# Performance work log

Measured on AMD Instinct MI355X. Metric: run time of the kernel, lower is better.

The kernel has to match this reference:

```python
import jax, jax.numpy as jnp
import numpy as np

B, L, T = 16, 256, 256
ENC, DEC, MEL, SPK = 256, 1024, 80, 256
ATT, FILT, K = 128, 32, 31


def setup_inputs() -> dict:
    key = jax.random.key(0)
    ks = jax.random.split(key, 32)
    s = 0.05
    r = lambda k, shape: jax.random.normal(k, shape, dtype=jnp.float32) * s
    return {
        'encoder_outputs': jax.random.normal(ks[0], (B, L, ENC), dtype=jnp.float32),
        'speaker_embed': jax.random.normal(ks[1], (B, SPK), dtype=jnp.float32),
        'mels': jax.random.normal(ks[2], (B, T, MEL), dtype=jnp.float32),
        # prenet
        'W_pre1': r(ks[3], (DEC, MEL)), 'b_pre1': jnp.zeros((DEC,), jnp.float32),
        'W_pre2': r(ks[4], (DEC, DEC)), 'b_pre2': jnp.zeros((DEC,), jnp.float32),
        # speaker projection
        'W_sp': r(ks[5], (DEC, SPK)), 'b_sp': jnp.zeros((DEC,), jnp.float32),
        # location-sensitive attention (Tacotron-2 style)
        'W_q': r(ks[6], (ATT, DEC)),
        'W_m': r(ks[7], (ATT, ENC)),
        'W_loc_conv': r(ks[8], (FILT, 2, K)),
        'W_loc': r(ks[9], (ATT, FILT)),
        'v_att': r(ks[10], (ATT,)),
        # LSTM cells
        'W_ih1': r(ks[11], (4 * DEC, DEC + ENC)), 'W_hh1': r(ks[12], (4 * DEC, DEC)),
        'b_ih1': jnp.zeros((4 * DEC,), jnp.float32), 'b_hh1': jnp.zeros((4 * DEC,), jnp.float32),
        'W_ih2': r(ks[13], (4 * DEC, DEC)), 'W_hh2': r(ks[14], (4 * DEC, DEC)),
        'b_ih2': jnp.zeros((4 * DEC,), jnp.float32), 'b_hh2': jnp.zeros((4 * DEC,), jnp.float32),
        # output projections
        'W_mel': r(ks[15], (MEL, DEC)), 'b_mel': jnp.zeros((MEL,), jnp.float32),
        'W_stop': r(ks[16], (1, DEC)), 'b_stop': jnp.zeros((1,), jnp.float32),
    }


def _lstm_cell(x, h, c, W_ih, W_hh, b_ih, b_hh):
    g = x @ W_ih.T + h @ W_hh.T + b_ih + b_hh
    i, f, gg, o = jnp.split(g, 4, axis=-1)
    c2 = jax.nn.sigmoid(f) * c + jax.nn.sigmoid(i) * jnp.tanh(gg)
    h2 = jax.nn.sigmoid(o) * jnp.tanh(c2)
    return h2, c2


def reference(encoder_outputs, speaker_embed, mels,
              W_pre1, b_pre1, W_pre2, b_pre2, W_sp, b_sp,
              W_q, W_m, W_loc_conv, W_loc, v_att,
              W_ih1, W_hh1, b_ih1, b_hh1, W_ih2, W_hh2, b_ih2, b_hh2,
              W_mel, b_mel, W_stop, b_stop):
    b = encoder_outputs.shape[0]
    proc_mem = jnp.einsum('bld,ad->bla', encoder_outputs, W_m)  # [B,L,ATT]
    spk = speaker_embed @ W_sp.T + b_sp                          # [B,DEC]
    # teacher forcing: step 0 uses zeros, step i>0 uses mels[:, i] (matches torch loop)
    prev_mel_seq = jnp.concatenate([jnp.zeros_like(mels[:, :1]), mels[:, 1:]], axis=1)
    prev_mel_seq = prev_mel_seq.transpose(1, 0, 2)               # [T,B,MEL]

    def step(carry, prev_mel):
        h1, c1, h2, c2, prev_w, cum_w = carry
        # prenet (dropout = identity in eval)
        p = jax.nn.relu(prev_mel @ W_pre1.T + b_pre1)
        p = jax.nn.relu(p @ W_pre2.T + b_pre2)
        q = p + spk
        # location features over [prev, cumulative] attention weights
        loc = jnp.stack([prev_w, cum_w], axis=1)                 # [B,2,L]
        f = jax.lax.conv_general_dilated(loc, W_loc_conv, (1,), [(K // 2, K // 2)],
                                         dimension_numbers=('NCH', 'OIH', 'NCH'))  # [B,FILT,L]
        e = jnp.einsum('bla,a->bl', jnp.tanh((q @ W_q.T)[:, None, :]
                                             + jnp.einsum('bcl,ac->bla', f, W_loc)
                                             + proc_mem), v_att)  # [B,L]
        w = jax.nn.softmax(e, axis=1)
        ctx = jnp.einsum('bl,bld->bd', w, encoder_outputs)        # [B,ENC]
        h1n, c1n = _lstm_cell(jnp.concatenate([p, ctx], axis=1), h1, c1, W_ih1, W_hh1, b_ih1, b_hh1)
        h2n, c2n = _lstm_cell(h1n, h2, c2, W_ih2, W_hh2, b_ih2, b_hh2)
        mel = h2n @ W_mel.T + b_mel
        stop = jax.nn.sigmoid(h2n @ W_stop.T + b_stop)
        return (h1n, c1n, h2n, c2n, w, cum_w + w), (mel, stop)

    z = lambda d: jnp.zeros((b, d), jnp.float32)
    carry0 = (z(DEC), z(DEC), z(DEC), z(DEC), z(L), z(L))
    _, (mel_seq, stop_seq) = jax.lax.scan(step, carry0, prev_mel_seq)
    return mel_seq.transpose(1, 0, 2), stop_seq.transpose(1, 0, 2)
```

## Files before the change

kernel.cpp:

```cpp
#include <hip/hip_runtime.h>


namespace {

constexpr int TT = 256, BB = 16, LL = 256, MELD = 80, FILTD = 32, KC = 31;
constexpr int P1 = 2304;
constexpr int P2 = 2048;
constexpr int REDOFF = 32768;

typedef float f32x4 __attribute__((ext_vector_type(4)));

struct Args {
  const float *enc, *spe, *mels;
  const float *Wpre1, *bpre1, *Wpre2, *bpre2, *Wsp, *bsp;
  const float *Wq, *Wm, *Wconv, *Wloc, *vatt;
  const float *Wih1, *Whh1, *bih1, *bhh1;
  const float *Wih2, *Whh2, *bih2, *bhh2;
  const float *Wmel, *bmel, *Wstop, *bstop;
  float *p, *X, *qp2, *pm2, *prevmel;
  float *h1a, *h1b, *c1, *h2a, *h2b, *c2;
  float *cum, *wexp, *uctx, *pctx, *psum, *spkvec, *spkq;
  float *W81, *b81, *tmp;
  int *slots, *epoch, *pslots, *pepoch;
  float *out;
};

__device__ __forceinline__ float fast_tanh(float x) {
  float ax = fabsf(x);
  float e = __expf(-2.f * ax);
  float t = (1.f - e) / (1.f + e);
  return copysignf(t, x);
}
__device__ __forceinline__ float fast_sig(float x) { return 1.f / (1.f + __expf(-x)); }

__device__ __forceinline__ int cldi(const int* p) {
  int v;
  asm volatile("global_load_dword %0, %1, off sc0 sc1\n\ts_waitcnt vmcnt(0)"
               : "=v"(v) : "v"(p) : "memory");
  return v;
}
__device__ __forceinline__ void cst1(float* p, float v) {
  asm volatile("global_store_dword %0, %1, off sc0 sc1" :: "v"(p), "v"(v) : "memory");
}
__device__ __forceinline__ void csti(int* p, int v) {
  asm volatile("global_store_dword %0, %1, off sc0 sc1" :: "v"(p), "v"(v) : "memory");
}
__device__ __forceinline__ void cld2(float* d0, float* d1, const float* q0,
                                     const float* q1) {
  float x, y;
  asm volatile(
      "global_load_dword %0, %2, off sc0 sc1\n\t"
      "global_load_dword %1, %3, off sc0 sc1\n\t"
      "s_waitcnt vmcnt(0)"
      : "=&v"(x), "=&v"(y) : "v"(q0), "v"(q1) : "memory");
  *d0 = x; *d1 = y;
}
__device__ __forceinline__ void cld4(f32x4 d[4], const f32x4* q0, const f32x4* q1,
                                     const f32x4* q2, const f32x4* q3) {
  asm volatile(
      "global_load_dwordx4 %0, %4, off sc0 sc1\n\t"
      "global_load_dwordx4 %1, %5, off sc0 sc1\n\t"
      "global_load_dwordx4 %2, %6, off sc0 sc1\n\t"
      "global_load_dwordx4 %3, %7, off sc0 sc1\n\t"
      "s_waitcnt vmcnt(0)"
      : "=&v"(d[0]), "=&v"(d[1]), "=&v"(d[2]), "=&v"(d[3])
      : "v"(q0), "v"(q1), "v"(q2), "v"(q3)
      : "memory");
}
__device__ __forceinline__ void cld8d(float d[8], const float* q0, const float* q1,
                                      const float* q2, const float* q3, const float* q4,
                                      const float* q5, const float* q6, const float* q7) {
  asm volatile(
      "global_load_dword %0, %8, off sc0 sc1\n\t"
      "global_load_dword %1, %9, off sc0 sc1\n\t"
      "global_load_dword %2, %10, off sc0 sc1\n\t"
      "global_load_dword %3, %11, off sc0 sc1\n\t"
      "global_load_dword %4, %12, off sc0 sc1\n\t"
      "global_load_dword %5, %13, off sc0 sc1\n\t"
      "global_load_dword %6, %14, off sc0 sc1\n\t"
      "global_load_dword %7, %15, off sc0 sc1\n\t"
      "s_waitcnt vmcnt(0)"
      : "=&v"(d[0]), "=&v"(d[1]), "=&v"(d[2]), "=&v"(d[3]),
        "=&v"(d[4]), "=&v"(d[5]), "=&v"(d[6]), "=&v"(d[7])
      : "v"(q0), "v"(q1), "v"(q2), "v"(q3), "v"(q4), "v"(q5), "v"(q6), "v"(q7)
      : "memory");
}

__device__ __forceinline__ void bar_lgkm() {
  asm volatile("s_waitcnt lgkmcnt(0)" ::: "memory");
  __builtin_amdgcn_s_barrier();
  __builtin_amdgcn_sched_barrier(0);
}

__device__ __forceinline__ void glls_c(const float* g, float* l) {
  __builtin_amdgcn_global_load_lds((const __attribute__((address_space(1))) void*)g,
                                   (__attribute__((address_space(3))) void*)l, 16, 0, 17);
}
__device__ __forceinline__ void glls_p(const float* g, float* l) {
  __builtin_amdgcn_global_load_lds((const __attribute__((address_space(1))) void*)g,
                                   (__attribute__((address_space(3))) void*)l, 16, 0, 0);
}

__device__ __forceinline__ void gridbar(int* slots, int* epoch, int target) {
  __syncthreads();
  if (blockIdx.x == 0) {
    if (threadIdx.x == 0) csti(&slots[0], target);
    while (cldi(&slots[threadIdx.x * 32]) < target) __builtin_amdgcn_s_sleep(1);
    __syncthreads();
    if (threadIdx.x == 0) csti(epoch, target);
  } else {
    if (threadIdx.x == 0) {
      csti(&slots[blockIdx.x * 32], target);
      while (cldi(epoch) < target) __builtin_amdgcn_s_sleep(8);
    }
  }
  __syncthreads();
}

__global__ void k_init(float* base, int n) {
  int i = blockIdx.x * blockDim.x + threadIdx.x;
  if (i < n) base[i] = 0.f;
}

__global__ void k_setpsum(float* psum) {
  if (threadIdx.x < 16) psum[256 + threadIdx.x * 16] = 1.f;
}

__global__ void k_prevmel(Args a) {
  int i = blockIdx.x * blockDim.x + threadIdx.x;
  if (i >= TT * BB * MELD) return;
  int m = i % MELD;
  int tb = i / MELD;
  int b = tb & 15, t = tb >> 4;
  a.prevmel[i] = (t == 0) ? 0.f : a.mels[(b * TT + t) * MELD + m];
}

__global__ void k_spkvec(Args a) {
  int i = blockIdx.x * blockDim.x + threadIdx.x;
  if (i >= BB * 1024) return;
  int b = i >> 10, j = i & 1023;
  const float* x = a.spe + b * 256;
  const float* w = a.Wsp + j * 256;
  float s = a.bsp[j];
  for (int k = 0; k < 256; ++k) s += x[k] * w[k];
  a.spkvec[i] = s;
}

__global__ void k_spkq(Args a) {
  int i = blockIdx.x * blockDim.x + threadIdx.x;
  if (i >= BB * 128) return;
  int b = i >> 7, q = i & 127;
  const float* x = a.spkvec + b * 1024;
  const float* w = a.Wq + q * 1024;
  float s = 0.f;
  for (int k = 0; k < 1024; ++k) s += x[k] * w[k];
  a.spkq[i] = s;
}

__global__ void k_prep81(Args a) {
  int i = blockIdx.x * blockDim.x + threadIdx.x;
  if (i < 81 * 1024) {
    int r = i >> 10, k = i & 1023;
    a.W81[i] = (r < 80) ? a.Wmel[r * 1024 + k] : a.Wstop[k];
  }
  if (i < 81) a.b81[i] = (i < 80) ? a.bmel[i] : a.bstop[0];
}

__global__ __launch_bounds__(256) void k_gemm(const float* __restrict__ A,
                                              const float* __restrict__ Bm,
                                              const float* __restrict__ bias,
                                              float* __restrict__ C,
                                              int M, int N, int K, int act) {
  __shared__ __align__(16) float As[16][132];
  __shared__ __align__(16) float Bs[16][68];
  const int bm = blockIdx.y * 128, bn = blockIdx.x * 64;
  const int tid = threadIdx.x;
  const int tm = (tid >> 4) * 8, tn = (tid & 15) * 4;
  float acc[8][4] = {};
  for (int k0 = 0; k0 < K; k0 += 16) {
    for (int i = tid; i < 512; i += 256) {
      int m = i >> 2, kq = i & 3;
      float4 v = *(const float4*)(A + (size_t)(bm + m) * K + k0 + kq * 4);
      As[kq * 4 + 0][m] = v.x; As[kq * 4 + 1][m] = v.y;
      As[kq * 4 + 2][m] = v.z; As[kq * 4 + 3][m] = v.w;
    }
    {
      int m = tid >> 2, kq = tid & 3;
      float4 v = *(const float4*)(Bm + (size_t)(bn + m) * K + k0 + kq * 4);
      Bs[kq * 4 + 0][m] = v.x; Bs[kq * 4 + 1][m] = v.y;
      Bs[kq * 4 + 2][m] = v.z; Bs[kq * 4 + 3][m] = v.w;
    }
    __syncthreads();
#pragma unroll
    for (int kk = 0; kk < 16; ++kk) {
      float4 a0 = *(const float4*)&As[kk][tm];
      float4 a1 = *(const float4*)&As[kk][tm + 4];
      float4 b0 = *(const float4*)&Bs[kk][tn];
      float av[8] = {a0.x, a0.y, a0.z, a0.w, a1.x, a1.y, a1.z, a1.w};
      float bv[4] = {b0.x, b0.y, b0.z, b0.w};
#pragma unroll
      for (int i = 0; i < 8; ++i)
#pragma unroll
        for (int j = 0; j < 4; ++j) acc[i][j] += av[i] * bv[j];
    }
    __syncthreads();
  }
#pragma unroll
  for (int i = 0; i < 8; ++i)
#pragma unroll
    for (int j = 0; j < 4; ++j) {
      float v = acc[i][j];
      if (bias) v += bias[bn + tn + j];
      if (act == 1) v = fmaxf(v, 0.f);
      C[(size_t)(bm + tm + i) * N + bn + tn + j] = v;
    }
}

__global__ void k_pm_transpose(Args a) {
  int i = blockIdx.x * blockDim.x + threadIdx.x;
  if (i >= BB * 128 * LL) return;
  int l = i & 255;
  int rest = i >> 8;
  int q = rest & 127, b = rest >> 7;
  a.pm2[i] = a.X[(size_t)((b << 8) + l) * 128 + q];
}

__global__ void k_addspkq(Args a) {
  int i = blockIdx.x * blockDim.x + threadIdx.x;
  if (i >= TT * BB * 128) return;
  int q = i & 127, b = (i >> 7) & 15;
  a.qp2[i] += a.spkq[b * 128 + q];
}

__global__ __launch_bounds__(256, 1) void k_persist(Args a) {
  __shared__ __align__(16) float xs[16 * P1];
  __shared__ __align__(16) float asc[720];
  __shared__ __align__(16) float gbuf2[280];
  __shared__ __align__(16) float wfb[2048];
  const int wg = blockIdx.x, tid = threadIdx.x;
  const int wv = tid >> 6, lane = tid & 63;
  const int d0 = wg * 4, kl = lane * 4;
  const int ag = tid & 15, ll = tid >> 4;

  float* loc0 = asc;
  float* loc1 = asc + 64;
  float* aF   = asc + 128;
  float* expv = asc + 704;

  float4 wL1[9][4];
  float4 wL2[8][4];
#pragma unroll
  for (int q = 0; q < 4; ++q) {
    const int row = wv * 1024 + d0 + q;
    const float* rih1 = a.Wih1 + (size_t)row * 1280;
    const float* rhh1 = a.Whh1 + (size_t)row * 1024;
    const float* rih2 = a.Wih2 + (size_t)row * 1024;
    const float* rhh2 = a.Whh2 + (size_t)row * 1024;
#pragma unroll
    for (int kb = 0; kb < 9; ++kb)
      wL1[kb][q] = (kb < 5) ? *(const float4*)(rih1 + kb * 256 + kl)
                            : *(const float4*)(rhh1 + kb * 256 + kl - 1280);
#pragma unroll
    for (int kb = 0; kb < 8; ++kb)
      wL2[kb][q] = (kb < 4) ? *(const float4*)(rih2 + kb * 256 + kl)
                            : *(const float4*)(rhh2 + kb * 256 + kl - 1024);
  }
  const int row_r = wv * 1024 + d0 + (lane >> 4);
  const float bsum1 = a.bih1[row_r] + a.bhh1[row_r];
  const float bsum2 = a.bih2[row_r] + a.bhh2[row_r];

  const int bH = wg >> 4, cH = wg & 15, l0H = cH << 4, lH = l0H + ll;
  float pmv[8], va[8];
  {
    const float* pmb = a.pm2 + (size_t)bH * 32768;
#pragma unroll
    for (int j = 0; j < 8; ++j) {
      pmv[j] = pmb[(size_t)(ag * 8 + j) * 256 + lH];
      va[j] = a.vatt[ag * 8 + j];
    }
  }
  float ev[16];
  {
    const float* eb = a.enc + (size_t)((bH << 8) + l0H) * 256 + tid;
#pragma unroll
    for (int l2 = 0; l2 < 16; ++l2) ev[l2] = eb[l2 * 256];
  }

  float c1v = 0.f, c2v = 0.f;
  __syncthreads();

  for (int t = 0; t < 259; ++t) {
    const int cur = t & 1, prv = cur ^ 1;

    if (wg < 16 && t >= 1 && t <= 256) {
      const int par = (t - 1) & 1, b = wg;
      float sm;
      {
        const f32x4* ps4 = (const f32x4*)(a.psum + par * 256 + b * 16);
        f32x4 pd[4];
        cld4(pd, ps4, ps4 + 1, ps4 + 2, ps4 + 3);
        sm = 0.f;
#pragma unroll
        for (int i = 0; i < 4; ++i) sm += pd[i][0] + pd[i][1] + pd[i][2] + pd[i][3];
      }
      const float inv = 1.f / sm;
      const float* pc = a.pctx + par * 65536 + b * 4096 + tid;
      float d[8];
      float acc = 0.f;
      cld8d(d, pc, pc + 256, pc + 512, pc + 768, pc + 1024, pc + 1280, pc + 1536,
            pc + 1792);
#pragma unroll
      for (int i = 0; i < 8; ++i) acc += d[i];
      cld8d(d, pc + 2048, pc + 2304, pc + 2560, pc + 2816, pc + 3072, pc + 3328,
            pc + 3584, pc + 3840);
#pragma unroll
      for (int i = 0; i < 8; ++i) acc += d[i];
      cst1(a.uctx + par * 4096 + b * 256 + tid, acc * inv);
    }

    float qv[8];
    if (t < 256) {
      float sm;
      {
        const f32x4* ps4 = (const f32x4*)(a.psum + prv * 256 + bH * 16);
        f32x4 pd[4];
        cld4(pd, ps4, ps4 + 1, ps4 + 2, ps4 + 3);
        sm = 0.f;
#pragma unroll
        for (int i = 0; i < 4; ++i) sm += pd[i][0] + pd[i][1] + pd[i][2] + pd[i][3];
      }
      const float inv_ps = 1.f / sm;
      {
        const float* qpb = a.qp2 + ((size_t)(t << 4) + bH) * 128 + ag * 8;
        *(float4*)&qv[0] = *(const float4*)qpb;
        *(float4*)&qv[4] = *(const float4*)(qpb + 4);
      }
      if (tid < 64) {
        int lp = l0H - 16 + tid;
        bool ok = (lp >= 0 && lp < LL);
        float we = 0.f, cm = 0.f;
        if (ok)
          cld2(&we, &cm, a.wexp + prv * 4096 + bH * 256 + lp,
               a.cum + prv * 4096 + bH * 256 + lp);
        float wn = we * inv_ps;
        loc0[tid] = wn;
        loc1[tid] = ok ? (cm + wn) : 0.f;
      }
      bar_lgkm();
      if (tid < 16) cst1(a.cum + cur * 4096 + bH * 256 + l0H + tid, loc1[16 + tid]);
      for (int idx = tid; idx < FILTD * 16; idx += 256) {
        int fc = idx >> 4, ll2 = idx & 15;
        const float* w = a.Wconv + fc * 62;
        float s = 0.f;
#pragma unroll
        for (int k = 0; k < KC; ++k) {
          s += w[k] * loc0[ll2 + k + 1];
          s += w[31 + k] * loc1[ll2 + k + 1];
        }
        aF[ll2 * 36 + fc] = s;
      }
      bar_lgkm();
      {
        const float* ftr = aF + ll * 36;
#pragma unroll
        for (int j = 0; j < 8; ++j) {
          const int r = ag * 8 + j;
          const float* wl = a.Wloc + r * 32;
          float x = 0.f;
#pragma unroll
          for (int c4 = 0; c4 < 8; ++c4) {
            float4 w4 = *(const float4*)(wl + c4 * 4);
            f32x4 f4 = *(const f32x4*)(ftr + c4 * 4);
            x += w4.x * f4[0] + w4.y * f4[1] + w4.z * f4[2] + w4.w * f4[3];
          }
          wfb[r * 16 + ll] = x;
        }
      }
    }

    if (t >= 2 && t <= 257) {
      const int s1 = t - 2;
      const float* pt = a.p + (size_t)s1 * 16384;
      const float* h1r = (s1 & 1) ? a.h1a : a.h1b;
      const float* uc = a.uctx + (size_t)(s1 & 1) * 4096;
#pragma unroll
      for (int k = 0; k < 16; ++k)
        glls_p(pt + (size_t)(tid + k * 256) * 4, xs + k * P1 + wv * 256);
#pragma unroll
      for (int k = 0; k < 4; ++k)
        glls_c(uc + (size_t)(tid + k * 256) * 4, xs + (k * 4 + wv) * P1 + 1024);
#pragma unroll
      for (int k = 0; k < 16; ++k)
        glls_c(h1r + (size_t)(tid + k * 256) * 4, xs + k * P1 + 1280 + wv * 256);
    }

    if (t < 256) {
      bar_lgkm();
      {
        float s = 0.f;
#pragma unroll
        for (int j = 0; j < 8; ++j) {
          float x = qv[j] + pmv[j] + wfb[(ag * 8 + j) * 16 + ll];
          s += va[j] * fast_tanh(x);
        }
        s += __shfl_down(s, 8, 16);
        s += __shfl_down(s, 4, 16);
        s += __shfl_down(s, 2, 16);
        s += __shfl_down(s, 1, 16);
        if (ag == 0) {
          float ex = __expf(s);
          expv[ll] = ex;
          cst1(a.wexp + cur * 4096 + bH * 256 + lH, ex);
        }
      }
      bar_lgkm();
      if (tid == 0) {
        float s = 0.f;
#pragma unroll
        for (int i = 0; i < 16; ++i) s += expv[i];
        cst1(a.psum + cur * 256 + bH * 16 + cH, s);
      }
      {
        float sctx = 0.f;
#pragma unroll
        for (int l2 = 0; l2 < 16; ++l2) sctx += expv[l2] * ev[l2];
        cst1(a.pctx + cur * 65536 + (bH * 16 + cH) * 256 + tid, sctx);
      }
    }

    if (t >= 2 && t <= 257) {
      __syncthreads();
      float acc[4][16];
#pragma unroll
      for (int q = 0; q < 4; ++q)
#pragma unroll
        for (int b = 0; b < 16; ++b) acc[q][b] = 0.f;
#pragma unroll
      for (int kb = 0; kb < 9; ++kb) {
        const float* xb = xs + kb * 256 + kl;
#pragma unroll
        for (int b = 0; b < 16; ++b) {
          float4 x4 = *(const float4*)(xb + b * P1);
#pragma unroll
          for (int q = 0; q < 4; ++q) {
            acc[q][b] += wL1[kb][q].x * x4.x;
            acc[q][b] += wL1[kb][q].y * x4.y;
            acc[q][b] += wL1[kb][q].z * x4.z;
            acc[q][b] += wL1[kb][q].w * x4.w;
          }
        }
      }
#pragma unroll
      for (int q = 0; q < 4; ++q)
#pragma unroll
        for (int b = 0; b < 16; ++b) {
          float v = acc[q][b];
          v += __shfl_xor(v, 32);
          v += __shfl_xor(v, 16);
          acc[q][b] = v;
        }
      if (lane < 16) {
        float* rb = xs + REDOFF + wv * 1024 + lane * 64;
        const int sx = lane << 2;
#pragma unroll
        for (int q = 0; q < 4; ++q)
#pragma unroll
          for (int bg = 0; bg < 4; ++bg) {
            f32x4 v = {acc[q][bg * 4 + 0], acc[q][bg * 4 + 1],
                       acc[q][bg * 4 + 2], acc[q][bg * 4 + 3]};
            *(f32x4*)(rb + ((q * 16 + bg * 4) ^ sx)) = v;
          }
      }
    }
    bar_lgkm();

    if (t >= 3) {
      const int s2 = t - 3;
      const float* h1s = (s2 & 1) ? a.h1b : a.h1a;
      const float* h2r = (s2 & 1) ? a.h2a : a.h2b;
#pragma unroll
      for (int k = 0; k < 16; ++k)
        glls_c(h1s + (size_t)(tid + k * 256) * 4, xs + k * P2 + wv * 256);
#pragma unroll
      for (int k = 0; k < 16; ++k)
        glls_c(h2r + (size_t)(tid + k * 256) * 4, xs + k * P2 + 1024 + wv * 256);
    }

    if (t >= 2 && t <= 257) {
      float* h1w = ((t - 2) & 1) ? a.h1b : a.h1a;
      {
        const int lo = lane & ~3, li = lane & 3;
        const float* rbase = xs + REDOFF + wv * 1024;
        float g = bsum1;
#pragma unroll
        for (int k = 0; k < 16; ++k) g += rbase[k * 64 + (lo ^ (k << 2)) + li];
        gbuf2[wv * 68 + lane] = g;
      }
      bar_lgkm();
      if (tid < 64) {
        int dd = tid >> 4, b = tid & 15, d = d0 + dd;
        float gi = gbuf2[0 * 68 + tid], gf = gbuf2[1 * 68 + tid];
        float gg = gbuf2[2 * 68 + tid], go = gbuf2[3 * 68 + tid];
        float cn = fast_sig(gf) * c1v + fast_sig(gi) * fast_tanh(gg);
        float hn = fast_sig(go) * fast_tanh(cn);
        c1v = cn;
        cst1(h1w + b * 1024 + d, hn);
      }
    }

    if (t >= 3) {
      const int s2 = t - 3;
      float* h2w = (s2 & 1) ? a.h2b : a.h2a;
      __syncthreads();
      float acc[4][16];
#pragma unroll
      for (int q = 0; q < 4; ++q)
#pragma unroll
        for (int b = 0; b < 16; ++b) acc[q][b] = 0.f;
#pragma unroll
      for (int kb = 0; kb < 8; ++kb) {
        const float* xb = xs + kb * 256 + kl;
#pragma unroll
        for (int b = 0; b < 16; ++b) {
          float4 x4 = *(const float4*)(xb + b * P2);
#pragma unroll
          for (int q = 0; q < 4; ++q) {
            acc[q][b] += wL2[kb][q].x * x4.x;
            acc[q][b] += wL2[kb][q].y * x4.y;
            acc[q][b] += wL2[kb][q].z * x4.z;
            acc[q][b] += wL2[kb][q].w * x4.w;
          }
        }
      }
#pragma unroll
      for (int q = 0; q < 4; ++q)
#pragma unroll
        for (int b = 0; b < 16; ++b) {
          float v = acc[q][b];
          v += __shfl_xor(v, 32);
          v += __shfl_xor(v, 16);
          acc[q][b] = v;
        }
      if (lane < 16) {
        float* rb = xs + REDOFF + wv * 1024 + lane * 64;
        const int sx = lane << 2;
#pragma unroll
        for (int q = 0; q < 4; ++q)
#pragma unroll
          for (int bg = 0; bg < 4; ++bg) {
            f32x4 v = {acc[q][bg * 4 + 0], acc[q][bg * 4 + 1],
                       acc[q][bg * 4 + 2], acc[q][bg * 4 + 3]};
            *(f32x4*)(rb + ((q * 16 + bg * 4) ^ sx)) = v;
          }
      }
      bar_lgkm();
      {
        const int lo = lane & ~3, li = lane & 3;
        const float* rbase = xs + REDOFF + wv * 1024;
        float g = bsum2;
#pragma unroll
        for (int k = 0; k < 16; ++k) g += rbase[k * 64 + (lo ^ (k << 2)) + li];
        gbuf2[wv * 68 + lane] = g;
      }
      bar_lgkm();
      if (tid < 64) {
        int dd = tid >> 4, b = tid & 15, d = d0 + dd;
        float gi = gbuf2[0 * 68 + tid], gf = gbuf2[1 * 68 + tid];
        float gg = gbuf2[2 * 68 + tid], go = gbuf2[3 * 68 + tid];
        float cn = fast_sig(gf) * c2v + fast_sig(gi) * fast_tanh(gg);
        float hn = fast_sig(go) * fast_tanh(cn);
        c2v = cn;
        cst1(h2w + b * 1024 + d, hn);
        a.X[(size_t)(s2 * 16 + b) * 1024 + d] = hn;
      }
    }

    if (t < 258) gridbar(a.slots, a.epoch, t + 1);
  }
}

__global__ void k_finish(Args a) {
  int i = blockIdx.x * blockDim.x + threadIdx.x;
  if (i >= 4096 * 128) return;
  int col = i & 127, tb = i >> 7;
  int t = tb >> 4, b = tb & 15;
  float v = a.tmp[i];
  if (col < 80) a.out[(size_t)(b * 256 + t) * 80 + col] = v;
  else if (col == 80) a.out[327680 + b * 256 + t] = fast_sig(v);
}

}

extern "C" void kernel_launch(void* const* d_in, const int* in_sizes, int n_in,
                              void* d_out, int out_size, void* d_ws, size_t ws_size,
                              hipStream_t stream) {
  float* ws = (float*)d_ws;
  Args a;
  a.enc = (const float*)d_in[0];
  a.spe = (const float*)d_in[1];
  a.mels = (const float*)d_in[2];
  a.Wpre1 = (const float*)d_in[3];  a.bpre1 = (const float*)d_in[4];
  a.Wpre2 = (const float*)d_in[5];  a.bpre2 = (const float*)d_in[6];
  a.Wsp = (const float*)d_in[7];    a.bsp = (const float*)d_in[8];
  a.Wq = (const float*)d_in[9];     a.Wm = (const float*)d_in[10];
  a.Wconv = (const float*)d_in[11]; a.Wloc = (const float*)d_in[12];
  a.vatt = (const float*)d_in[13];
  a.Wih1 = (const float*)d_in[14];  a.Whh1 = (const float*)d_in[15];
  a.bih1 = (const float*)d_in[16];  a.bhh1 = (const float*)d_in[17];
  a.Wih2 = (const float*)d_in[18];  a.Whh2 = (const float*)d_in[19];
  a.bih2 = (const float*)d_in[20];  a.bhh2 = (const float*)d_in[21];
  a.Wmel = (const float*)d_in[22];  a.bmel = (const float*)d_in[23];
  a.Wstop = (const float*)d_in[24]; a.bstop = (const float*)d_in[25];

  a.p    = ws + 0;
  a.X    = ws + 4194304;
  a.qp2  = ws + 8388608;
  a.pm2  = ws + 8912896;
  float* st = ws + 9437184;
  a.h1a = st + 0;      a.h1b = st + 16384;
  a.c1  = st + 32768;
  a.h2a = st + 49152;  a.h2b = st + 65536;
  a.c2  = st + 81920;
  a.cum  = st + 98304;
  a.wexp = st + 106496;
  a.uctx = st + 114688;
  a.pctx = st + 122880;
  a.psum = st + 253952;
  a.slots  = (int*)(st + 254464);
  a.epoch  = (int*)(st + 262656);
  a.pslots = (int*)(st + 262688);
  a.pepoch = (int*)(st + 270880);
  a.spkvec = ws + 9708096;
  a.spkq   = ws + 9724480;
  a.W81    = ws + 9726528;
  a.b81    = ws + 9857600;
  a.tmp    = ws + 9857728;
  a.prevmel = a.tmp;
  a.out = (float*)d_out;

  k_init<<<(270912 + 255) / 256, 256, 0, stream>>>(st, 270912);
  k_setpsum<<<1, 64, 0, stream>>>(a.psum);
  k_prevmel<<<(TT * BB * MELD + 255) / 256, 256, 0, stream>>>(a);
  k_spkvec<<<(BB * 1024 + 255) / 256, 256, 0, stream>>>(a);
  k_spkq<<<(BB * 128 + 255) / 256, 256, 0, stream>>>(a);
  k_prep81<<<(81 * 1024 + 255) / 256, 256, 0, stream>>>(a);

  k_gemm<<<dim3(16, 32), 256, 0, stream>>>(a.prevmel, a.Wpre1, a.bpre1, a.X, 4096, 1024, 80, 1);
  k_gemm<<<dim3(16, 32), 256, 0, stream>>>(a.X, a.Wpre2, a.bpre2, a.p, 4096, 1024, 1024, 1);
  k_gemm<<<dim3(2, 32), 256, 0, stream>>>(a.p, a.Wq, nullptr, a.qp2, 4096, 128, 1024, 0);
  k_addspkq<<<(TT * BB * 128 + 255) / 256, 256, 0, stream>>>(a);
  k_gemm<<<dim3(2, 32), 256, 0, stream>>>(a.enc, a.Wm, nullptr, a.X, 4096, 128, 256, 0);
  k_pm_transpose<<<(BB * 128 * LL + 255) / 256, 256, 0, stream>>>(a);

  {
    void* kargs[] = {(void*)&a};
    hipError_t e = hipLaunchCooperativeKernel(reinterpret_cast<const void*>(&k_persist),
                                              dim3(256), dim3(256), kargs, 0, stream);
    if (e != hipSuccess) k_persist<<<256, 256, 0, stream>>>(a);
  }

  k_gemm<<<dim3(2, 32), 256, 0, stream>>>(a.X, a.W81, a.b81, a.tmp, 4096, 128, 1024, 0);
  k_finish<<<(4096 * 128 + 255) / 256, 256, 0, stream>>>(a);
}
```

Baseline: 14.30 ms.

## Replace coherent per-load cache bypass with acquire fence, keep attention features in registers

Drops the sc0/sc1 coherent inline-asm loads and the cache-bypassing global_load_lds variants. Visibility of cross-block data is now handled by a single agent-scope acquire fence after each grid barrier, so ordinary loads can be cached and scheduled by the compiler. The location-feature projection result now stays in registers (wf) instead of going through an LDS buffer, which removes that buffer and one block barrier. Another barrier is moved before the reduction store and one after it is removed. This risks memory-ordering or LDS race bugs if the fence or barrier placement is not sufficient.

After: 15.37 ms. +7.5%, slower.

```diff
diff --git a/kernel.cpp b/kernel.cpp
--- a/kernel.cpp
+++ b/kernel.cpp
@@ -45,46 +45,6 @@
 __device__ __forceinline__ void csti(int* p, int v) {
   asm volatile("global_store_dword %0, %1, off sc0 sc1" :: "v"(p), "v"(v) : "memory");
 }
-__device__ __forceinline__ void cld2(float* d0, float* d1, const float* q0,
-                                     const float* q1) {
-  float x, y;
-  asm volatile(
-      "global_load_dword %0, %2, off sc0 sc1\n\t"
-      "global_load_dword %1, %3, off sc0 sc1\n\t"
-      "s_waitcnt vmcnt(0)"
-      : "=&v"(x), "=&v"(y) : "v"(q0), "v"(q1) : "memory");
-  *d0 = x; *d1 = y;
-}
-__device__ __forceinline__ void cld4(f32x4 d[4], const f32x4* q0, const f32x4* q1,
-                                     const f32x4* q2, const f32x4* q3) {
-  asm volatile(
-      "global_load_dwordx4 %0, %4, off sc0 sc1\n\t"
-      "global_load_dwordx4 %1, %5, off sc0 sc1\n\t"
-      "global_load_dwordx4 %2, %6, off sc0 sc1\n\t"
-      "global_load_dwordx4 %3, %7, off sc0 sc1\n\t"
-      "s_waitcnt vmcnt(0)"
-      : "=&v"(d[0]), "=&v"(d[1]), "=&v"(d[2]), "=&v"(d[3])
-      : "v"(q0), "v"(q1), "v"(q2), "v"(q3)
-      : "memory");
-}
-__device__ __forceinline__ void cld8d(float d[8], const float* q0, const float* q1,
-                                      const float* q2, const float* q3, const float* q4,
-                                      const float* q5, const float* q6, const float* q7) {
-  asm volatile(
-      "global_load_dword %0, %8, off sc0 sc1\n\t"
-      "global_load_dword %1, %9, off sc0 sc1\n\t"
-      "global_load_dword %2, %10, off sc0 sc1\n\t"
-      "global_load_dword %3, %11, off sc0 sc1\n\t"
-      "global_load_dword %4, %12, off sc0 sc1\n\t"
-      "global_load_dword %5, %13, off sc0 sc1\n\t"
-      "global_load_dword %6, %14, off sc0 sc1\n\t"
-      "global_load_dword %7, %15, off sc0 sc1\n\t"
-      "s_waitcnt vmcnt(0)"
-      : "=&v"(d[0]), "=&v"(d[1]), "=&v"(d[2]), "=&v"(d[3]),
-        "=&v"(d[4]), "=&v"(d[5]), "=&v"(d[6]), "=&v"(d[7])
-      : "v"(q0), "v"(q1), "v"(q2), "v"(q3), "v"(q4), "v"(q5), "v"(q6), "v"(q7)
-      : "memory");
-}
 
 __device__ __forceinline__ void bar_lgkm() {
   asm volatile("s_waitcnt lgkmcnt(0)" ::: "memory");
@@ -92,11 +52,7 @@
   __builtin_amdgcn_sched_barrier(0);
 }
 
-__device__ __forceinline__ void glls_c(const float* g, float* l) {
-  __builtin_amdgcn_global_load_lds((const __attribute__((address_space(1))) void*)g,
-                                   (__attribute__((address_space(3))) void*)l, 16, 0, 17);
-}
-__device__ __forceinline__ void glls_p(const float* g, float* l) {
+__device__ __forceinline__ void glls(const float* g, float* l) {
   __builtin_amdgcn_global_load_lds((const __attribute__((address_space(1))) void*)g,
                                    (__attribute__((address_space(3))) void*)l, 16, 0, 0);
 }
@@ -114,6 +70,7 @@
       while (cldi(epoch) < target) __builtin_amdgcn_s_sleep(8);
     }
   }
+  __builtin_amdgcn_fence(__ATOMIC_ACQUIRE, "agent");
   __syncthreads();
 }
 
@@ -236,7 +193,6 @@
   __shared__ __align__(16) float xs[16 * P1];
   __shared__ __align__(16) float asc[720];
   __shared__ __align__(16) float gbuf2[280];
-  __shared__ __align__(16) float wfb[2048];
   const int wg = blockIdx.x, tid = threadIdx.x;
   const int wv = tid >> 6, lane = tid & 63;
   const int d0 = wg * 4, kl = lane * 4;
@@ -297,51 +253,45 @@
       float sm;
       {
         const f32x4* ps4 = (const f32x4*)(a.psum + par * 256 + b * 16);
-        f32x4 pd[4];
-        cld4(pd, ps4, ps4 + 1, ps4 + 2, ps4 + 3);
-        sm = 0.f;
-#pragma unroll
-        for (int i = 0; i < 4; ++i) sm += pd[i][0] + pd[i][1] + pd[i][2] + pd[i][3];
+        f32x4 p0 = ps4[0], p1 = ps4[1], p2 = ps4[2], p3 = ps4[3];
+        sm = (p0[0] + p0[1] + p0[2] + p0[3]) + (p1[0] + p1[1] + p1[2] + p1[3]) +
+             (p2[0] + p2[1] + p2[2] + p2[3]) + (p3[0] + p3[1] + p3[2] + p3[3]);
       }
       const float inv = 1.f / sm;
       const float* pc = a.pctx + par * 65536 + b * 4096 + tid;
-      float d[8];
       float acc = 0.f;
-      cld8d(d, pc, pc + 256, pc + 512, pc + 768, pc + 1024, pc + 1280, pc + 1536,
-            pc + 1792);
-#pragma unroll
-      for (int i = 0; i < 8; ++i) acc += d[i];
-      cld8d(d, pc + 2048, pc + 2304, pc + 2560, pc + 2816, pc + 3072, pc + 3328,
-            pc + 3584, pc + 3840);
-#pragma unroll
-      for (int i = 0; i < 8; ++i) acc += d[i];
+#pragma unroll
+      for (int i = 0; i < 16; ++i) acc += pc[i * 256];
       cst1(a.uctx + par * 4096 + b * 256 + tid, acc * inv);
     }
 
-    float qv[8];
+    float qpm[8], wf[8];
     if (t < 256) {
       float sm;
       {
         const f32x4* ps4 = (const f32x4*)(a.psum + prv * 256 + bH * 16);
-        f32x4 pd[4];
-        cld4(pd, ps4, ps4 + 1, ps4 + 2, ps4 + 3);
-        sm = 0.f;
-#pragma unroll
-        for (int i = 0; i < 4; ++i) sm += pd[i][0] + pd[i][1] + pd[i][2] + pd[i][3];
+        f32x4 p0 = ps4[0], p1 = ps4[1], p2 = ps4[2], p3 = ps4[3];
+        sm = (p0[0] + p0[1] + p0[2] + p0[3]) + (p1[0] + p1[1] + p1[2] + p1[3]) +
+             (p2[0] + p2[1] + p2[2] + p2[3]) + (p3[0] + p3[1] + p3[2] + p3[3]);
       }
       const float inv_ps = 1.f / sm;
       {
         const float* qpb = a.qp2 + ((size_t)(t << 4) + bH) * 128 + ag * 8;
-        *(float4*)&qv[0] = *(const float4*)qpb;
-        *(float4*)&qv[4] = *(const float4*)(qpb + 4);
+        float4 q0 = *(const float4*)qpb;
+        float4 q1 = *(const float4*)(qpb + 4);
+        qpm[0] = q0.x + pmv[0]; qpm[1] = q0.y + pmv[1];
+        qpm[2] = q0.z + pmv[2]; qpm[3] = q0.w + pmv[3];
+        qpm[4] = q1.x + pmv[4]; qpm[5] = q1.y + pmv[5];
+        qpm[6] = q1.z + pmv[6]; qpm[7] = q1.w + pmv[7];
       }
       if (tid < 64) {
         int lp = l0H - 16 + tid;
         bool ok = (lp >= 0 && lp < LL);
         float we = 0.f, cm = 0.f;
-        if (ok)
-          cld2(&we, &cm, a.wexp + prv * 4096 + bH * 256 + lp,
-               a.cum + prv * 4096 + bH * 256 + lp);
+        if (ok) {
+          we = a.wexp[prv * 4096 + bH * 256 + lp];
+          cm = a.cum[prv * 4096 + bH * 256 + lp];
+        }
         float wn = we * inv_ps;
         loc0[tid] = wn;
         loc1[tid] = ok ? (cm + wn) : 0.f;
@@ -362,18 +312,19 @@
       bar_lgkm();
       {
         const float* ftr = aF + ll * 36;
+        f32x4 f[8];
+#pragma unroll
+        for (int c4 = 0; c4 < 8; ++c4) f[c4] = *(const f32x4*)(ftr + c4 * 4);
 #pragma unroll
         for (int j = 0; j < 8; ++j) {
-          const int r = ag * 8 + j;
-          const float* wl = a.Wloc + r * 32;
+          const float* wl = a.Wloc + (ag * 8 + j) * 32;
           float x = 0.f;
 #pragma unroll
           for (int c4 = 0; c4 < 8; ++c4) {
             float4 w4 = *(const float4*)(wl + c4 * 4);
-            f32x4 f4 = *(const f32x4*)(ftr + c4 * 4);
-            x += w4.x * f4[0] + w4.y * f4[1] + w4.z * f4[2] + w4.w * f4[3];
+            x += w4.x * f[c4][0] + w4.y * f[c4][1] + w4.z * f[c4][2] + w4.w * f[c4][3];
           }
-          wfb[r * 16 + ll] = x;
+          wf[j] = x;
         }
       }
     }
@@ -385,24 +336,20 @@
       const float* uc = a.uctx + (size_t)(s1 & 1) * 4096;
 #pragma unroll
       for (int k = 0; k < 16; ++k)
-        glls_p(pt + (size_t)(tid + k * 256) * 4, xs + k * P1 + wv * 256);
+        glls(pt + (size_t)(tid + k * 256) * 4, xs + k * P1 + wv * 256);
 #pragma unroll
       for (int k = 0; k < 4; ++k)
-        glls_c(uc + (size_t)(tid + k * 256) * 4, xs + (k * 4 + wv) * P1 + 1024);
+        glls(uc + (size_t)(tid + k * 256) * 4, xs + (k * 4 + wv) * P1 + 1024);
 #pragma unroll
       for (int k = 0; k < 16; ++k)
-        glls_c(h1r + (size_t)(tid + k * 256) * 4, xs + k * P1 + 1280 + wv * 256);
+        glls(h1r + (size_t)(tid + k * 256) * 4, xs + k * P1 + 1280 + wv * 256);
     }
 
     if (t < 256) {
-      bar_lgkm();
       {
         float s = 0.f;
 #pragma unroll
-        for (int j = 0; j < 8; ++j) {
-          float x = qv[j] + pmv[j] + wfb[(ag * 8 + j) * 16 + ll];
-          s += va[j] * fast_tanh(x);
-        }
+        for (int j = 0; j < 8; ++j) s += va[j] * fast_tanh(qpm[j] + wf[j]);
         s += __shfl_down(s, 8, 16);
         s += __shfl_down(s, 4, 16);
         s += __shfl_down(s, 2, 16);
@@ -459,6 +406,7 @@
           v += __shfl_xor(v, 16);
           acc[q][b] = v;
         }
+      bar_lgkm();
       if (lane < 16) {
         float* rb = xs + REDOFF + wv * 1024 + lane * 64;
         const int sx = lane << 2;
@@ -472,7 +420,6 @@
           }
       }
     }
-    bar_lgkm();
 
     if (t >= 3) {
       const int s2 = t - 3;
@@ -480,10 +427,10 @@
       const float* h2r = (s2 & 1) ? a.h2a : a.h2b;
 #pragma unroll
       for (int k = 0; k < 16; ++k)
-        glls_c(h1s + (size_t)(tid + k * 256) * 4, xs + k * P2 + wv * 256);
+        glls(h1s + (size_t)(tid + k * 256) * 4, xs + k * P2 + wv * 256);
 #pragma unroll
       for (int k = 0; k < 16; ++k)
-        glls_c(h2r + (size_t)(tid + k * 256) * 4, xs + k * P2 + 1024 + wv * 256);
+        glls(h2r + (size_t)(tid + k * 256) * 4, xs + k * P2 + 1024 + wv * 256);
     }
 
     if (t >= 2 && t <= 257) {
@@ -553,7 +500,6 @@
             *(f32x4*)(rb + ((q * 16 + bg * 4) ^ sx)) = v;
           }
       }
-      bar_lgkm();
       {
         const int lo = lane & ~3, li = lane & 3;
         const float* rbase = xs + REDOFF + wv * 1024;
```
